# Kernel optimization log

Hardware: AMD Instinct MI355X
Metric: run time of the kernel (lower is better)

## Reference

```python
import jax, jax.numpy as jnp
import numpy as np

N = 100000
E = 1600000
IN_DIM = 256
HID = 128


def gcn_conv(x, edge_index, W, b):
    # x: [N, F_in], edge_index: [2, E] (row=source, col=target)
    h = x @ W  # [N, F_out]
    n = x.shape[0]
    loops = jnp.arange(n, dtype=edge_index.dtype)
    row = jnp.concatenate([edge_index[0], loops])
    col = jnp.concatenate([edge_index[1], loops])
    w = jnp.ones(row.shape[0], dtype=h.dtype)
    deg = jax.ops.segment_sum(w, col, num_segments=n)
    dinv = jnp.where(deg > 0, jax.lax.rsqrt(deg), 0.0)
    norm = dinv[row] * dinv[col]  # [E+N]
    msgs = h[row] * norm[:, None]  # gather + scale
    out = jax.ops.segment_sum(msgs, col, num_segments=n)  # scatter-add at targets
    return out + b


def setup_inputs() -> dict:
    key = jax.random.key(0)
    ks = jax.random.split(key, 8)
    x = jax.random.normal(ks[0], (N, IN_DIM), dtype=jnp.float32)
    edge_index = jax.random.randint(ks[1], (2, E), 0, N, dtype=jnp.int64)
    s1 = 1.0 / np.sqrt(IN_DIM)
    s2 = 1.0 / np.sqrt(HID)
    W1 = jax.random.uniform(ks[2], (IN_DIM, HID), jnp.float32, -s1, s1)
    b1 = jnp.zeros((HID,), jnp.float32)
    W2 = jax.random.uniform(ks[3], (HID, HID), jnp.float32, -s2, s2)
    b2 = jnp.zeros((HID,), jnp.float32)
    Wp = jax.random.uniform(ks[4], (HID, HID), jnp.float32, -s2, s2)
    bp = jax.random.uniform(ks[5], (HID,), jnp.float32, -s2, s2)
    return {"x": x, "edge_index": edge_index, "W1": W1, "b1": b1,
            "W2": W2, "b2": b2, "Wp": Wp, "bp": bp}


def reference(x, edge_index, W1, b1, W2, b2, Wp, bp):
    # Faithful GConv.forward with conv='gcn': two GCNConv layers (no
    # activation/dropout/norm applied in the original forward), then a
    # linear projection head; returns (z, projection(z)).
    z = gcn_conv(x, edge_index, W1, b1)
    z = gcn_conv(z, edge_index, W2, b2)
    proj = z @ Wp + bp
    return (z, proj)
```

## Files before the change

### kernel.cpp

```cpp
#include <hip/hip_runtime.h>

typedef __attribute__((ext_vector_type(8))) short short8;
typedef __attribute__((ext_vector_type(4))) float f32x4;

__device__ __forceinline__ float bf2f(unsigned short u) {
    union { unsigned int i; float f; } v; v.i = ((unsigned int)u) << 16; return v.f;
}
__device__ __forceinline__ unsigned short f2bf(float f) {
    union { float f; unsigned int i; } v; v.f = f;
    unsigned int i = v.i;
    return (unsigned short)((i + 0x7FFFu + ((i >> 16) & 1u)) >> 16);
}
__device__ __forceinline__ float ldext(const void* p, size_t i, int xf) {
    return xf ? ((const float*)p)[i] : bf2f(((const unsigned short*)p)[i]);
}
__device__ __forceinline__ float scrub(float v) {
    return (__builtin_fabsf(v) < 1e30f) ? v : 9.0f;
}

__global__ void k_detect(const int* __restrict__ ei, const unsigned short* __restrict__ xs,
                         int* __restrict__ flags) {
    int lane = threadIdx.x;
    int orv = 0;
    for (int i = 2 * lane + 1; i < 256; i += 128) orv |= ei[i];
    int cnt = 0;
    for (int i = lane; i < 256; i += 64) {
        int e = (xs[i] >> 7) & 0xFF;
        cnt += (e >= 97 && e <= 159) ? 1 : 0;
    }
    for (int off = 32; off > 0; off >>= 1) {
        orv |= __shfl_down(orv, off);
        cnt += __shfl_down(cnt, off);
    }
    if (lane == 0) {
        flags[0] = (orv == 0) ? 1 : 0;
        flags[1] = (cnt >= 240) ? 0 : 1;
    }
}

#define BSH 10
#define BNODES (1 << BSH)
#define RBITS (32 - BSH)
#define EPB 16

__global__ void k_zero(int* __restrict__ p, int n) {
    int i = blockIdx.x * 256 + threadIdx.x;
    if (i < n) p[i] = 0;
}

__global__ __launch_bounds__(256) void k_bcount(const int* __restrict__ ei,
                                                const int* __restrict__ flags,
                                                int* __restrict__ bcnt,
                                                int e, int n, int nb) {
    __shared__ int hist[1024];
    int tid = threadIdx.x;
    for (int i = tid; i < 1024; i += 256) hist[i] = 0;
    __syncthreads();
    int f = flags[0];
    long base = (long)blockIdx.x * (256 * EPB);
#pragma unroll
    for (int j = 0; j < EPB; ++j) {
        long i = base + j * 256 + tid;
        if (i < e) {
            int c = ei[(e + i) << f];
            if ((unsigned)c >= (unsigned)n) c = 0;
            atomicAdd(&hist[c >> BSH], 1);
        }
    }
    __syncthreads();
    for (int b = tid; b < nb; b += 256) {
        int h = hist[b];
        if (h) atomicAdd(&bcnt[b], h);
    }
}

__global__ __launch_bounds__(1024) void k_bscan(const int* __restrict__ bcnt,
                                                int* __restrict__ boff,
                                                int* __restrict__ bcur,
                                                int nb, int e,
                                                int* __restrict__ rowptr, int n) {
    __shared__ int ws[16];
    int t = threadIdx.x, lane = t & 63, wv = t >> 6;
    int v = (t < nb) ? bcnt[t] : 0;
    int s = v;
    for (int off = 1; off < 64; off <<= 1) {
        int x = __shfl_up(s, off);
        if (lane >= off) s += x;
    }
    if (lane == 63) ws[wv] = s;
    __syncthreads();
    if (wv == 0 && lane < 16) {
        int w = ws[lane];
        for (int off = 1; off < 16; off <<= 1) {
            int x = __shfl_up(w, off);
            if (lane >= off) w += x;
        }
        ws[lane] = w;
    }
    __syncthreads();
    int excl = (wv ? ws[wv - 1] : 0) + s - v;
    if (t < nb) { boff[t] = excl; bcur[t] = excl; }
    if (t == 0) { boff[nb] = e; rowptr[n] = e; }
}

__global__ __launch_bounds__(256) void k_bin(const int* __restrict__ ei,
                                             const int* __restrict__ flags,
                                             int* __restrict__ bcur,
                                             int* __restrict__ binned,
                                             int e, int n, int nb) {
    __shared__ int hist[1024];
    __shared__ int wbase[1024];
    int tid = threadIdx.x;
    for (int i = tid; i < 1024; i += 256) hist[i] = 0;
    __syncthreads();
    int f = flags[0];
    long base = (long)blockIdx.x * (256 * EPB);
    int cs[EPB], rr[EPB];
#pragma unroll
    for (int j = 0; j < EPB; ++j) {
        long i = base + j * 256 + tid;
        int c = -1, r = 0;
        if (i < e) {
            c = ei[(e + i) << f];
            r = ei[i << f];
            if ((unsigned)c >= (unsigned)n) c = 0;
            if ((unsigned)r >= (unsigned)n) r = 0;
            atomicAdd(&hist[c >> BSH], 1);
        }
        cs[j] = c;
        rr[j] = r;
    }
    __syncthreads();
    for (int b = tid; b < nb; b += 256) {
        int h = hist[b];
        wbase[b] = h ? atomicAdd(&bcur[b], h) : 0;
    }
    __syncthreads();
    for (int i = tid; i < 1024; i += 256) hist[i] = 0;
    __syncthreads();
#pragma unroll
    for (int j = 0; j < EPB; ++j) {
        int c = cs[j];
        if (c >= 0) {
            int b = c >> BSH;
            int off = atomicAdd(&hist[b], 1);
            int rec = rr[j] | ((c & (BNODES - 1)) << RBITS);
            binned[wbase[b] + off] = rec;
        }
    }
}

__global__ __launch_bounds__(256) void k_build(const int* __restrict__ binned,
                                               const int* __restrict__ boff,
                                               int* __restrict__ rowptr,
                                               float* __restrict__ dinv,
                                               int* __restrict__ csr_src,
                                               int n) {
    __shared__ int hist[1024];
    __shared__ int ws4[4];
    int b = blockIdx.x;
    int tid = threadIdx.x;
    int v0 = b << BSH;
    int rs = boff[b], re = boff[b + 1];
    for (int i = tid; i < 1024; i += 256) hist[i] = 0;
    __syncthreads();
    for (int i = rs + tid; i < re; i += 256)
        atomicAdd(&hist[((unsigned)binned[i]) >> RBITS], 1);
    __syncthreads();
    int idx = tid * 4;
    int h0 = hist[idx], h1 = hist[idx + 1], h2 = hist[idx + 2], h3 = hist[idx + 3];
    int ls = h0 + h1 + h2 + h3;
    int lane = tid & 63, wv = tid >> 6;
    int s = ls;
    for (int off = 1; off < 64; off <<= 1) {
        int x = __shfl_up(s, off);
        if (lane >= off) s += x;
    }
    if (lane == 63) ws4[wv] = s;
    __syncthreads();
    int wb = 0;
    for (int k = 0; k < 4; ++k) wb += (k < wv) ? ws4[k] : 0;
    int excl = wb + (s - ls);
    int e0 = excl, e1 = excl + h0, e2 = e1 + h1, e3 = e2 + h2;
    hist[idx] = rs + e0; hist[idx + 1] = rs + e1;
    hist[idx + 2] = rs + e2; hist[idx + 3] = rs + e3;
    int vv = v0 + idx;
    if (vv < n)     { rowptr[vv]     = rs + e0; dinv[vv]     = rsqrtf((float)(h0 + 1)); }
    if (vv + 1 < n) { rowptr[vv + 1] = rs + e1; dinv[vv + 1] = rsqrtf((float)(h1 + 1)); }
    if (vv + 2 < n) { rowptr[vv + 2] = rs + e2; dinv[vv + 2] = rsqrtf((float)(h2 + 1)); }
    if (vv + 3 < n) { rowptr[vv + 3] = rs + e3; dinv[vv + 3] = rsqrtf((float)(h3 + 1)); }
    __syncthreads();
    for (int i = rs + tid; i < re; i += 256) {
        int rec = binned[i];
        int cl = ((unsigned)rec) >> RBITS;
        int r = rec & ((1 << RBITS) - 1);
        int pos = atomicAdd(&hist[cl], 1);
        csr_src[pos] = r;
    }
}


__global__ __launch_bounds__(256) void k_wprep(const void* __restrict__ W,
                                               short8* __restrict__ Wf,
                                               int K, const int* __restrict__ flags) {
    int idx = blockIdx.x * 256 + threadIdx.x;
    int total = (K >> 5) * 8 * 64;
    if (idx >= total) return;
    int lane = idx & 63, frow = idx >> 6;
    int t = frow & 7, ksg = frow >> 3;
    int col = t * 16 + (lane & 15);
    int k0 = ksg * 32 + ((lane >> 4) << 3);
    int xf = flags[1];
    short8 val;
    if (xf) {
        const float* wp = (const float*)W + (size_t)k0 * 128 + col;
#pragma unroll
        for (int j = 0; j < 8; ++j) val[j] = (short)f2bf(wp[(size_t)j * 128]);
    } else {
        const unsigned short* wp = (const unsigned short*)W + (size_t)k0 * 128 + col;
#pragma unroll
        for (int j = 0; j < 8; ++j) val[j] = (short)wp[(size_t)j * 128];
    }
    Wf[idx] = val;
}

__device__ __forceinline__ short8 load_frag(const void* A, size_t row, int K, int off, int f32m) {
    if (!f32m)
        return *(const short8*)((const unsigned short*)A + row * (size_t)K + off);
    const float* p = (const float*)A + row * (size_t)K + off;
    short8 r;
#pragma unroll
    for (int j = 0; j < 8; ++j) r[j] = (short)f2bf(p[j]);
    return r;
}

__global__ __launch_bounds__(256) void k_gemm(
    const void* __restrict__ A, const short8* __restrict__ Wf,
    void* __restrict__ Cbase, const void* __restrict__ bias,
    int M, int K, const int* __restrict__ flags,
    int a_ext, int c_half, int c_ext) {
    int xf = flags[1];
    int af = a_ext & xf;
    int cf = c_ext & xf;
    char* cp = (char*)Cbase + (size_t)c_half * (size_t)M * 128 * (xf ? 4 : 2);

    int tid = threadIdx.x;
    int wave = tid >> 6, lane = tid & 63;
    int quad = lane >> 4, l16 = lane & 15;
    int row0 = (blockIdx.x * 4 + wave) * 32;
    if (row0 >= M) return;

    f32x4 acc[2][8];
#pragma unroll
    for (int m = 0; m < 2; ++m)
#pragma unroll
        for (int t = 0; t < 8; ++t)
            acc[m][t] = (f32x4){0.f, 0.f, 0.f, 0.f};

    size_t ar0 = (size_t)min(row0 + l16, M - 1);
    size_t ar1 = (size_t)min(row0 + 16 + l16, M - 1);

    int nks = K >> 5;
#pragma unroll 2
    for (int ksg = 0; ksg < nks; ++ksg) {
        int k0 = (ksg << 5) + quad * 8;
        short8 a0 = load_frag(A, ar0, K, k0, af);
        short8 a1 = load_frag(A, ar1, K, k0, af);
        const short8* wrow = Wf + (size_t)(ksg << 3) * 64 + lane;
#pragma unroll
        for (int t = 0; t < 8; ++t) {
            short8 bf = wrow[t * 64];
            acc[0][t] = __builtin_amdgcn_mfma_f32_16x16x32_bf16(a0, bf, acc[0][t], 0, 0, 0);
            acc[1][t] = __builtin_amdgcn_mfma_f32_16x16x32_bf16(a1, bf, acc[1][t], 0, 0, 0);
        }
    }
#pragma unroll
    for (int t = 0; t < 8; ++t) {
        int colx = t * 16 + l16;
        float bv = bias ? ldext(bias, colx, xf) : 0.f;
#pragma unroll
        for (int m = 0; m < 2; ++m) {
#pragma unroll
            for (int r = 0; r < 4; ++r) {
                int row = row0 + m * 16 + quad * 4 + r;
                if (row < M) {
                    float v = scrub(acc[m][t][r] + bv);
                    if (cf) ((float*)cp)[(size_t)row * 128 + colx] = v;
                    else ((unsigned short*)cp)[(size_t)row * 128 + colx] = f2bf(v);
                }
            }
        }
    }
}


__global__ __launch_bounds__(256) void k_agg(
    const void* __restrict__ hbase, int h_half,
    const int* __restrict__ rowptr, const int* __restrict__ csr_src,
    const float* __restrict__ dinv, const void* __restrict__ bias,
    void* __restrict__ z, int z_ext,
    int n, int etot, const int* __restrict__ flags) {
    int v = (blockIdx.x * 256 + threadIdx.x) >> 4;
    if (v >= n) return;
    int xf = flags[1];
    int zf = z_ext & xf;
    const unsigned short* h = (const unsigned short*)
        ((const char*)hbase + (size_t)h_half * (size_t)n * 128 * (xf ? 4 : 2));
    int g = threadIdx.x & 15;
    float di = dinv[v];
    int s = rowptr[v], e = rowptr[v + 1];
    if (e > etot) e = etot;
    if (s < 0) s = 0;

    short8 hv = *(const short8*)(h + (size_t)v * 128 + g * 8);
    float sw = di * di;
    float acc[8];
#pragma unroll
    for (int j = 0; j < 8; ++j) acc[j] = bf2f((unsigned short)hv[j]) * sw;

    int u0 = (s < e) ? csr_src[s] : 0;
    if ((unsigned)u0 >= (unsigned)n) u0 = 0;
    float du0 = dinv[u0];
    short8 h0 = *(const short8*)(h + (size_t)u0 * 128 + g * 8);
    for (int i = s; i < e; ++i) {
        int u1 = (i + 1 < e) ? csr_src[i + 1] : 0;
        if ((unsigned)u1 >= (unsigned)n) u1 = 0;
        float du1 = dinv[u1];
        short8 h1 = *(const short8*)(h + (size_t)u1 * 128 + g * 8);
        float w = di * du0;
#pragma unroll
        for (int j = 0; j < 8; ++j) acc[j] += bf2f((unsigned short)h0[j]) * w;
        u0 = u1; du0 = du1; h0 = h1;
    }

#pragma unroll
    for (int j = 0; j < 8; ++j)
        acc[j] = scrub(acc[j] + ldext(bias, g * 8 + j, xf));

    if (zf) {
        float* zp = (float*)z + (size_t)v * 128 + g * 8;
        f32x4 o0 = {acc[0], acc[1], acc[2], acc[3]};
        f32x4 o1 = {acc[4], acc[5], acc[6], acc[7]};
        *(f32x4*)zp = o0;
        *(f32x4*)(zp + 4) = o1;
    } else {
        short8 o;
#pragma unroll
        for (int j = 0; j < 8; ++j) o[j] = (short)f2bf(acc[j]);
        *(short8*)((unsigned short*)z + (size_t)v * 128 + g * 8) = o;
    }
}


static inline size_t alignup(size_t x) { return (x + 255) & ~(size_t)255; }

extern "C" void kernel_launch(void* const* d_in, const int* in_sizes, int n_in,
                              void* d_out, int out_size, void* d_ws, size_t ws_size,
                              hipStream_t stream) {
    const void* x  = d_in[0];
    const int*  ei = (const int*)d_in[1];
    const void* W1 = d_in[2];
    const void* b1 = d_in[3];
    const void* W2 = d_in[4];
    const void* b2 = d_in[5];
    const void* Wp = d_in[6];
    const void* bp = d_in[7];

    const int HID = in_sizes[3];
    const int IN_DIM = in_sizes[2] / HID;
    const int N = in_sizes[0] / IN_DIM;
    const int E = in_sizes[1] / 2;

    char* w = (char*)d_ws;
    int* flags = (int*)w;      w += 256;
    int* rowptr = (int*)w;     w += alignup(sizeof(int) * (size_t)(N + 1));
    float* dinv = (float*)w;   w += alignup(sizeof(float) * (size_t)N);
    int* bcnt = (int*)w;       w += 4096;
    int* boff = (int*)w;       w += 8192;
    int* bcur = (int*)w;       w += 4096;
    short8* wf1 = (short8*)w;  w += alignup((size_t)IN_DIM * HID * 2);
    short8* wf2 = (short8*)w;  w += alignup((size_t)HID * HID * 2);
    short8* wfp = (short8*)w;  w += alignup((size_t)HID * HID * 2);
    int* csr_src = (int*)w;    w += alignup(sizeof(int) * (size_t)E);
    size_t fixed = (size_t)(w - (char*)d_ws);
    size_t bufbytes = alignup((size_t)N * HID * 2);
    bool wsmode = ws_size >= fixed + 2 * bufbytes;

    int* binned = (int*)d_out;

    void* hC;  int h_half;
    void* z1p;
    if (wsmode) {
        hC = (void*)w;  h_half = 0;
        z1p = (void*)(w + bufbytes);
    } else {
        hC = d_out;     h_half = 1;
        z1p = d_out;
    }

    int nb = (N + BNODES - 1) >> BSH;
    int ebb = (E + 256 * EPB - 1) / (256 * EPB);
    int tiles = (N + 31) / 32;
    int gemm_blocks = (tiles + 3) / 4;
    int agg_blocks = (N + 15) / 16;

    k_detect<<<1, 64, 0, stream>>>(ei, (const unsigned short*)x, flags);
    k_wprep<<<(IN_DIM * 16 + 255) / 256, 256, 0, stream>>>(W1, wf1, IN_DIM, flags);
    k_wprep<<<(HID * 16 + 255) / 256, 256, 0, stream>>>(W2, wf2, HID, flags);
    k_wprep<<<(HID * 16 + 255) / 256, 256, 0, stream>>>(Wp, wfp, HID, flags);
    k_zero<<<(nb + 255) / 256, 256, 0, stream>>>(bcnt, nb);
    k_bcount<<<ebb, 256, 0, stream>>>(ei, flags, bcnt, E, N, nb);
    k_bscan<<<1, 1024, 0, stream>>>(bcnt, boff, bcur, nb, E, rowptr, N);
    k_bin<<<ebb, 256, 0, stream>>>(ei, flags, bcur, binned, E, N, nb);
    k_build<<<nb, 256, 0, stream>>>(binned, boff, rowptr, dinv, csr_src, N);

    k_gemm<<<gemm_blocks, 256, 0, stream>>>(x, wf1, hC, nullptr, N, IN_DIM, flags,
                                            1, h_half, 0);
    k_agg<<<agg_blocks, 256, 0, stream>>>(hC, h_half, rowptr, csr_src, dinv, b1,
                                          z1p, 0, N, E, flags);

    k_gemm<<<gemm_blocks, 256, 0, stream>>>(z1p, wf2, hC, nullptr, N, HID, flags,
                                            0, h_half, 0);
    k_agg<<<agg_blocks, 256, 0, stream>>>(hC, h_half, rowptr, csr_src, dinv, b2,
                                          d_out, 1, N, E, flags);

    k_gemm<<<gemm_blocks, 256, 0, stream>>>(d_out, wfp, d_out, bp, N, HID, flags,
                                            1, 1, 1);
}
```

Baseline: 567.4 us.

## Template GEMM on K with preloaded A rows and double-buffered weight fragments

Replaces the generic GEMM with a kernel templated on K and on the input format. Each wave now handles 16 rows instead of 32. The whole A row strip is loaded into registers up front, using vectorized float4 loads when the input is fp32, and the weight fragments are double-buffered across k-steps. The aim is to overlap global loads with MFMA work and raise occupancy by running more, smaller tiles. The cost is that each weight fragment is reused across half as many rows, so weight traffic goes up, and register pressure rises from holding the full A strip.

```diff
diff --git a/kernel.cpp b/kernel.cpp
--- a/kernel.cpp
+++ b/kernel.cpp
@@ -16,6 +16,12 @@
 }
 __device__ __forceinline__ float scrub(float v) {
     return (__builtin_fabsf(v) < 1e30f) ? v : 9.0f;
+}
+__device__ __forceinline__ short8 as_short8(f32x4 v) {
+    union { f32x4 f; short8 s; } u; u.f = v; return u.s;
+}
+__device__ __forceinline__ f32x4 as_f32x4(short8 v) {
+    union { short8 s; f32x4 f; } u; u.s = v; return u.f;
 }
 
 __global__ void k_detect(const int* __restrict__ ei, const unsigned short* __restrict__ xs,
@@ -224,6 +230,92 @@
     Wf[idx] = val;
 }
 
+__device__ __forceinline__ void loadw(short8 (&w)[8], const short8* __restrict__ Wf,
+                                      int ksg, int lane) {
+#pragma unroll
+    for (int t = 0; t < 8; ++t) w[t] = Wf[(size_t)((ksg << 3) + t) * 64 + lane];
+}
+
+template<int AEXT>
+__device__ __forceinline__ short8 cvt_frag(short8 lo, short8 hi, int af) {
+    if (AEXT == 0) return lo;
+    if (!af) return lo;
+    f32x4 f0 = as_f32x4(lo), f1 = as_f32x4(hi);
+    short8 r;
+#pragma unroll
+    for (int j = 0; j < 4; ++j) {
+        r[j] = (short)f2bf(f0[j]);
+        r[j + 4] = (short)f2bf(f1[j]);
+    }
+    return r;
+}
+
+__device__ __forceinline__ void step8(f32x4 (&acc)[8], short8 a, short8 (&w)[8]) {
+#pragma unroll
+    for (int t = 0; t < 8; ++t)
+        acc[t] = __builtin_amdgcn_mfma_f32_16x16x32_bf16(a, w[t], acc[t], 0, 0, 0);
+}
+
+template<int NKS, int AEXT>
+__global__ __launch_bounds__(256) void k_gemmT(
+    const void* __restrict__ A, const short8* __restrict__ Wf,
+    void* __restrict__ Cbase, const void* __restrict__ bias,
+    int M, const int* __restrict__ flags, int c_half, int c_ext) {
+    const int K = NKS * 32;
+    int xf = flags[1];
+    int af = AEXT & xf;
+    int cf = c_ext & xf;
+    char* cp = (char*)Cbase + (size_t)c_half * (size_t)M * 128 * (xf ? 4 : 2);
+
+    int tid = threadIdx.x;
+    int wave = tid >> 6, lane = tid & 63;
+    int quad = lane >> 4, l16 = lane & 15;
+    int row0 = (blockIdx.x * 4 + wave) * 16;
+    if (row0 >= M) return;
+    size_t ar = (size_t)min(row0 + l16, M - 1);
+
+    short8 a_lo[NKS], a_hi[NKS];
+#pragma unroll
+    for (int k = 0; k < NKS; ++k) {
+        if (AEXT && af) {
+            const f32x4* p = (const f32x4*)((const float*)A + ar * (size_t)K + k * 32 + quad * 8);
+            a_lo[k] = as_short8(p[0]);
+            a_hi[k] = as_short8(p[1]);
+        } else {
+            a_lo[k] = *(const short8*)((const unsigned short*)A + ar * (size_t)K + k * 32 + quad * 8);
+        }
+    }
+
+    f32x4 acc[8];
+#pragma unroll
+    for (int t = 0; t < 8; ++t) acc[t] = (f32x4){0.f, 0.f, 0.f, 0.f};
+
+    short8 wA[8], wB[8];
+    loadw(wA, Wf, 0, lane);
+#pragma unroll
+    for (int kp = 0; kp < NKS; kp += 2) {
+        if (kp + 1 < NKS) loadw(wB, Wf, kp + 1, lane);
+        step8(acc, cvt_frag<AEXT>(a_lo[kp], a_hi[kp], af), wA);
+        if (kp + 2 < NKS) loadw(wA, Wf, kp + 2, lane);
+        if (kp + 1 < NKS) step8(acc, cvt_frag<AEXT>(a_lo[kp + 1], a_hi[kp + 1], af), wB);
+    }
+
+#pragma unroll
+    for (int t = 0; t < 8; ++t) {
+        int colx = t * 16 + l16;
+        float bv = bias ? ldext(bias, colx, xf) : 0.f;
+#pragma unroll
+        for (int r = 0; r < 4; ++r) {
+            int row = row0 + quad * 4 + r;
+            if (row < M) {
+                float v = scrub(acc[t][r] + bv);
+                if (cf) ((float*)cp)[(size_t)row * 128 + colx] = v;
+                else ((unsigned short*)cp)[(size_t)row * 128 + colx] = f2bf(v);
+            }
+        }
+    }
+}
+
 __device__ __forceinline__ short8 load_frag(const void* A, size_t row, int K, int off, int f32m) {
     if (!f32m)
         return *(const short8*)((const unsigned short*)A + row * (size_t)K + off);
@@ -234,7 +326,7 @@
     return r;
 }
 
-__global__ __launch_bounds__(256) void k_gemm(
+__global__ __launch_bounds__(256) void k_gemm_gen(
     const void* __restrict__ A, const short8* __restrict__ Wf,
     void* __restrict__ Cbase, const void* __restrict__ bias,
     int M, int K, const int* __restrict__ flags,
@@ -243,51 +335,34 @@
     int af = a_ext & xf;
     int cf = c_ext & xf;
     char* cp = (char*)Cbase + (size_t)c_half * (size_t)M * 128 * (xf ? 4 : 2);
-
     int tid = threadIdx.x;
     int wave = tid >> 6, lane = tid & 63;
     int quad = lane >> 4, l16 = lane & 15;
-    int row0 = (blockIdx.x * 4 + wave) * 32;
+    int row0 = (blockIdx.x * 4 + wave) * 16;
     if (row0 >= M) return;
-
-    f32x4 acc[2][8];
-#pragma unroll
-    for (int m = 0; m < 2; ++m)
+    size_t ar = (size_t)min(row0 + l16, M - 1);
+    f32x4 acc[8];
+#pragma unroll
+    for (int t = 0; t < 8; ++t) acc[t] = (f32x4){0.f, 0.f, 0.f, 0.f};
+    int nks = K >> 5;
+    for (int ksg = 0; ksg < nks; ++ksg) {
+        short8 a = load_frag(A, ar, K, (ksg << 5) + quad * 8, af);
+        const short8* wrow = Wf + (size_t)(ksg << 3) * 64 + lane;
 #pragma unroll
         for (int t = 0; t < 8; ++t)
-            acc[m][t] = (f32x4){0.f, 0.f, 0.f, 0.f};
-
-    size_t ar0 = (size_t)min(row0 + l16, M - 1);
-    size_t ar1 = (size_t)min(row0 + 16 + l16, M - 1);
-
-    int nks = K >> 5;
-#pragma unroll 2
-    for (int ksg = 0; ksg < nks; ++ksg) {
-        int k0 = (ksg << 5) + quad * 8;
-        short8 a0 = load_frag(A, ar0, K, k0, af);
-        short8 a1 = load_frag(A, ar1, K, k0, af);
-        const short8* wrow = Wf + (size_t)(ksg << 3) * 64 + lane;
-#pragma unroll
-        for (int t = 0; t < 8; ++t) {
-            short8 bf = wrow[t * 64];
-            acc[0][t] = __builtin_amdgcn_mfma_f32_16x16x32_bf16(a0, bf, acc[0][t], 0, 0, 0);
-            acc[1][t] = __builtin_amdgcn_mfma_f32_16x16x32_bf16(a1, bf, acc[1][t], 0, 0, 0);
-        }
+            acc[t] = __builtin_amdgcn_mfma_f32_16x16x32_bf16(a, wrow[t * 64], acc[t], 0, 0, 0);
     }
 #pragma unroll
     for (int t = 0; t < 8; ++t) {
         int colx = t * 16 + l16;
         float bv = bias ? ldext(bias, colx, xf) : 0.f;
 #pragma unroll
-        for (int m = 0; m < 2; ++m) {
-#pragma unroll
-            for (int r = 0; r < 4; ++r) {
-                int row = row0 + m * 16 + quad * 4 + r;
-                if (row < M) {
-                    float v = scrub(acc[m][t][r] + bv);
-                    if (cf) ((float*)cp)[(size_t)row * 128 + colx] = v;
-                    else ((unsigned short*)cp)[(size_t)row * 128 + colx] = f2bf(v);
-                }
+        for (int r = 0; r < 4; ++r) {
+            int row = row0 + quad * 4 + r;
+            if (row < M) {
+                float v = scrub(acc[t][r] + bv);
+                if (cf) ((float*)cp)[(size_t)row * 128 + colx] = v;
+                else ((unsigned short*)cp)[(size_t)row * 128 + colx] = f2bf(v);
             }
         }
     }
@@ -400,9 +475,21 @@
 
     int nb = (N + BNODES - 1) >> BSH;
     int ebb = (E + 256 * EPB - 1) / (256 * EPB);
-    int tiles = (N + 31) / 32;
-    int gemm_blocks = (tiles + 3) / 4;
+    int gemm_blocks = (N + 63) / 64;
     int agg_blocks = (N + 15) / 16;
+
+    auto launch_gemm = [&](const void* A, const short8* Wf, void* C, const void* bias,
+                           int K, int aext, int chalf, int cext) {
+        if (K == 256) {
+            if (aext) k_gemmT<8, 1><<<gemm_blocks, 256, 0, stream>>>(A, Wf, C, bias, N, flags, chalf, cext);
+            else      k_gemmT<8, 0><<<gemm_blocks, 256, 0, stream>>>(A, Wf, C, bias, N, flags, chalf, cext);
+        } else if (K == 128) {
+            if (aext) k_gemmT<4, 1><<<gemm_blocks, 256, 0, stream>>>(A, Wf, C, bias, N, flags, chalf, cext);
+            else      k_gemmT<4, 0><<<gemm_blocks, 256, 0, stream>>>(A, Wf, C, bias, N, flags, chalf, cext);
+        } else {
+            k_gemm_gen<<<gemm_blocks, 256, 0, stream>>>(A, Wf, C, bias, N, K, flags, aext, chalf, cext);
+        }
+    };
 
     k_detect<<<1, 64, 0, stream>>>(ei, (const unsigned short*)x, flags);
     k_wprep<<<(IN_DIM * 16 + 255) / 256, 256, 0, stream>>>(W1, wf1, IN_DIM, flags);
@@ -414,16 +501,13 @@
     k_bin<<<ebb, 256, 0, stream>>>(ei, flags, bcur, binned, E, N, nb);
     k_build<<<nb, 256, 0, stream>>>(binned, boff, rowptr, dinv, csr_src, N);
 
-    k_gemm<<<gemm_blocks, 256, 0, stream>>>(x, wf1, hC, nullptr, N, IN_DIM, flags,
-                                            1, h_half, 0);
+    launch_gemm(x, wf1, hC, nullptr, IN_DIM, 1, h_half, 0);
     k_agg<<<agg_blocks, 256, 0, stream>>>(hC, h_half, rowptr, csr_src, dinv, b1,
                                           z1p, 0, N, E, flags);
 
-    k_gemm<<<gemm_blocks, 256, 0, stream>>>(z1p, wf2, hC, nullptr, N, HID, flags,
-                                            0, h_half, 0);
+    launch_gemm(z1p, wf2, hC, nullptr, HID, 0, h_half, 0);
     k_agg<<<agg_blocks, 256, 0, stream>>>(hC, h_half, rowptr, csr_src, dinv, b2,
                                           d_out, 1, N, E, flags);
 
-    k_gemm<<<gemm_blocks, 256, 0, stream>>>(d_out, wfp, d_out, bp, N, HID, flags,
-                                            1, 1, 1);
-}
+    launch_gemm(d_out, wfp, d_out, bp, HID, 1, 1, 1);
+}
```

Measured after the change: 512.8 us. 9.6% less time.
